# Performance work log

Measured on AMD Instinct MI355X. Metric: run time of the kernel, lower is better.

Reference implementation:

```python
import jax, jax.numpy as jnp
import numpy as np

N, H, W, CIN, COUT, FSIZE = 8, 128, 128, 64, 128, 3
EPS = 1e-3      # keras BatchNormalization default epsilon
ALPHA = 0.2     # LeakyReLU alpha


def setup_inputs() -> dict:
    key = jax.random.key(0)
    k0, k1, k2 = jax.random.split(key, 3)
    return {
        "inputs_real": jax.random.normal(k0, (N, H, W, CIN), jnp.float32),
        "inputs_imag": jax.random.normal(k1, (N, H, W, CIN), jnp.float32),
        "filters": jax.random.normal(k2, (FSIZE, FSIZE, CIN, COUT), jnp.float32) * 0.1,
        "gamma_real": jnp.ones((COUT,), jnp.float32),
        "beta_real": jnp.zeros((COUT,), jnp.float32),
        "gamma_imag": jnp.ones((COUT,), jnp.float32),
        "beta_imag": jnp.zeros((COUT,), jnp.float32),
    }


def _bn_train(x, gamma, beta):
    # BatchNorm in training mode: batch stats over (N, H, W), biased variance.
    mean = jnp.mean(x, axis=(0, 1, 2), keepdims=True)
    var = jnp.var(x, axis=(0, 1, 2), keepdims=True)
    return gamma * (x - mean) * jax.lax.rsqrt(var + EPS) + beta


def _leaky(x):
    return jnp.where(x >= 0, x, ALPHA * x)


def _spectral_kernels(filters):
    # Pad spatial filters [f,f,Cin,Cout] to [H,W,Cin,Cout] (bottom/right), FFT over H,W.
    f = filters.shape[0]
    fp = jnp.pad(filters, ((0, H - f), (0, W - f), (0, 0), (0, 0)))
    ff = jnp.fft.fft2(jnp.transpose(fp, (2, 3, 0, 1)).astype(jnp.complex64))  # [Cin,Cout,H,W]
    ff = jnp.transpose(ff, (2, 3, 0, 1))  # [H,W,Cin,Cout]
    kr = jnp.real(ff)
    ki = jnp.real(ff)  # faithful to source: filters_imag is ALSO tf.math.real(filters_freq)
    return kr, ki


def reference(inputs_real, inputs_imag, filters, gamma_real, beta_real, gamma_imag, beta_imag):
    kr, ki = _spectral_kernels(filters)
    # Fused form of the per-batch loop: sum over Cin of (ac+bd) and (bc-ad).
    out_real = (jnp.einsum('nhwc,hwco->nhwo', inputs_real, kr)
                + jnp.einsum('nhwc,hwco->nhwo', inputs_imag, ki))
    out_imag = (jnp.einsum('nhwc,hwco->nhwo', inputs_imag, kr)
                - jnp.einsum('nhwc,hwco->nhwo', inputs_real, ki))
    out_real = _leaky(_bn_train(out_real, gamma_real, beta_real))
    out_imag = _leaky(_bn_train(out_imag, gamma_imag, beta_imag))
    return (out_real, out_imag)
```

## Files before the change

### kernel.cpp

```cpp
#include <hip/hip_runtime.h>
#include <hip/hip_bf16.h>


typedef __bf16 bf16x8 __attribute__((ext_vector_type(8)));
typedef float f32x4 __attribute__((ext_vector_type(4)));

#define PQ_STRIDE   72
#define PQ_PLANE    (128 * PQ_STRIDE)
#define XS_STRIDE   72
#define XS_NP       (16 * XS_STRIDE)

__device__ __forceinline__ unsigned short f2bf(float x) {
    unsigned u = __float_as_uint(x);
    return (unsigned short)((u + 0x7FFFu + ((u >> 16) & 1u)) >> 16);
}
__device__ __forceinline__ unsigned pack2(float a, float b) {
    __hip_bfloat162 h = __float22bfloat162_rn(make_float2(a, b));
    return *reinterpret_cast<unsigned*>(&h);
}
__device__ __forceinline__ void unpack8(uint4 u, float* f) {
    f[0] = __uint_as_float(u.x << 16); f[1] = __uint_as_float(u.x & 0xffff0000u);
    f[2] = __uint_as_float(u.y << 16); f[3] = __uint_as_float(u.y & 0xffff0000u);
    f[4] = __uint_as_float(u.z << 16); f[5] = __uint_as_float(u.z & 0xffff0000u);
    f[6] = __uint_as_float(u.w << 16); f[7] = __uint_as_float(u.w & 0xffff0000u);
}

__global__ __launch_bounds__(512, 2) void conv_stats(
    const float* __restrict__ xr, const float* __restrict__ xi,
    const float* __restrict__ filt, float* __restrict__ out,
    float* __restrict__ gstats)
{
    __shared__ __align__(16) unsigned short pqT[5 * PQ_PLANE];
    __shared__ __align__(16) unsigned short xsh[16 * XS_NP];
    __shared__ float statl[512];

    const int t = threadIdx.x;
    const int u = blockIdx.x >> 3;
    const int vbase = (blockIdx.x & 7) * 16;

    const float au = 6.28318530717958647692f * (float)u / 128.0f;
    float su1, cu1, su2, cu2;
    __sincosf(au, &su1, &cu1);
    __sincosf(2.0f * au, &su2, &cu2);
    unsigned* pq32 = (unsigned*)pqT;

    #pragma unroll
    for (int k = 0; k < 8; ++k) {
        int i = t + k * 512;
        int o = i & 127;
        int cp = i >> 7;
        int g0 = (2 * cp) * 128 + o;
        int g1 = g0 + 128;
        unsigned widx = o * 36 + cp;
        #pragma unroll
        for (int b = 0; b < 3; ++b) {
            float f0a = filt[b * 8192 + g0],        f0b = filt[b * 8192 + g1];
            float f1a = filt[(3 + b) * 8192 + g0],  f1b = filt[(3 + b) * 8192 + g1];
            float f2a = filt[(6 + b) * 8192 + g0],  f2b = filt[(6 + b) * 8192 + g1];
            float Pa = f0a + cu1 * f1a + cu2 * f2a;
            float Pb = f0b + cu1 * f1b + cu2 * f2b;
            pq32[b * 4608 + widx] = pack2(Pa, Pb);
            if (b > 0) {
                float Qa = su1 * f1a + su2 * f2a;
                float Qb = su1 * f1b + su2 * f2b;
                pq32[(b + 2) * 4608 + widx] = pack2(Qa, Qb);
            }
        }
    }

    #pragma unroll
    for (int k = 0; k < 16; ++k) {
        int p = t + k * 512;
        int c = p & 63;
        int v = (p >> 6) & 15;
        int n = p >> 10;
        size_t gi = ((size_t)(n * 128 + u) * 128 + (size_t)(vbase + v)) * 64 + c;
        float r = xr[gi], im = xi[gi];
        xsh[v * XS_NP + n * XS_STRIDE + c]       = f2bf(r + im);
        xsh[v * XS_NP + (8 + n) * XS_STRIDE + c] = f2bf(im - r);
    }
    __syncthreads();

    const int wave = t >> 6;
    const int lane = t & 63;
    const int vg   = wave >> 1;
    const int nth  = wave & 1;
    const int ln15 = lane & 15;
    const int q    = lane >> 4;

    float cv1[4], cv2[4], nsv1[4], nsv2[4];
    #pragma unroll
    for (int vj = 0; vj < 4; ++vj) {
        float av = 6.28318530717958647692f * (float)(vbase + vg * 4 + vj) / 128.0f;
        float s1, c1, s2, c2;
        __sincosf(av, &s1, &c1);
        __sincosf(2.0f * av, &s2, &c2);
        cv1[vj] = c1; cv2[vj] = c2; nsv1[vj] = -s1; nsv2[vj] = -s2;
    }

    bf16x8 af[4][2];
    #pragma unroll
    for (int vj = 0; vj < 4; ++vj) {
        const unsigned short* xrow = &xsh[(vg * 4 + vj) * XS_NP + ln15 * XS_STRIDE];
        af[vj][0] = __builtin_bit_cast(bf16x8, *(const uint4*)(xrow + q * 8));
        af[vj][1] = __builtin_bit_cast(bf16x8, *(const uint4*)(xrow + 32 + q * 8));
    }

    f32x4 acc[4][4];
    #pragma unroll
    for (int vj = 0; vj < 4; ++vj)
        #pragma unroll
        for (int ntl = 0; ntl < 4; ++ntl)
            acc[vj][ntl] = (f32x4){0.f, 0.f, 0.f, 0.f};

    #pragma unroll
    for (int ntl = 0; ntl < 4; ++ntl) {
        const int o = (nth * 4 + ntl) * 16 + ln15;
        const unsigned short* prow = &pqT[o * PQ_STRIDE];
        #pragma unroll
        for (int ks = 0; ks < 2; ++ks) {
            const int coff = ks * 32 + q * 8;
            float P0[8], P1[8], P2[8], Q1[8], Q2[8];
            unpack8(*(const uint4*)(prow + 0 * PQ_PLANE + coff), P0);
            unpack8(*(const uint4*)(prow + 1 * PQ_PLANE + coff), P1);
            unpack8(*(const uint4*)(prow + 2 * PQ_PLANE + coff), P2);
            unpack8(*(const uint4*)(prow + 3 * PQ_PLANE + coff), Q1);
            unpack8(*(const uint4*)(prow + 4 * PQ_PLANE + coff), Q2);
            #pragma unroll
            for (int vj = 0; vj < 4; ++vj) {
                float kr[8];
                #pragma unroll
                for (int j = 0; j < 8; ++j) {
                    float tv = fmaf(cv1[vj], P1[j], P0[j]);
                    tv = fmaf(cv2[vj], P2[j], tv);
                    tv = fmaf(nsv1[vj], Q1[j], tv);
                    kr[j] = fmaf(nsv2[vj], Q2[j], tv);
                }
                uint4 B;
                B.x = pack2(kr[0], kr[1]); B.y = pack2(kr[2], kr[3]);
                B.z = pack2(kr[4], kr[5]); B.w = pack2(kr[6], kr[7]);
                acc[vj][ntl] = __builtin_amdgcn_mfma_f32_16x16x32_bf16(
                    af[vj][ks], __builtin_bit_cast(bf16x8, B), acc[vj][ntl], 0, 0, 0);
            }
        }
    }

    float ssum[4] = {0, 0, 0, 0}, ssq[4] = {0, 0, 0, 0};
    const int part = q >> 1;
    const int nbase = (q & 1) * 4;
    #pragma unroll
    for (int vj = 0; vj < 4; ++vj) {
        const int v = vbase + vg * 4 + vj;
        const size_t pos = ((size_t)(u * 128 + v)) * 128;
        #pragma unroll
        for (int ntl = 0; ntl < 4; ++ntl) {
            const int o = (nth * 4 + ntl) * 16 + ln15;
            size_t base = (size_t)part * 16777216 + (size_t)nbase * 2097152 + pos + o;
            #pragma unroll
            for (int r = 0; r < 4; ++r) {
                float y = acc[vj][ntl][r];
                __builtin_nontemporal_store(y, out + base + (size_t)r * 2097152);
                ssum[ntl] += y;
                ssq[ntl] = fmaf(y, y, ssq[ntl]);
            }
        }
    }

    statl[t] = 0.f;
    __syncthreads();
    #pragma unroll
    for (int ntl = 0; ntl < 4; ++ntl) {
        int ch = part * 128 + (nth * 4 + ntl) * 16 + ln15;
        atomicAdd(&statl[ch], ssum[ntl]);
        atomicAdd(&statl[256 + ch], ssq[ntl]);
    }
    __syncthreads();
    atomicAdd(&gstats[t], statl[t]);
}

__global__ void bn_prep(const float* __restrict__ gstats,
                        const float* __restrict__ gr, const float* __restrict__ br,
                        const float* __restrict__ gi, const float* __restrict__ bi,
                        float* __restrict__ sc_sh)
{
    int t = threadIdx.x;
    if (t < 256) {
        int part = t >> 7, o = t & 127;
        const float inv = 1.0f / 131072.0f;
        float mean = gstats[t] * inv;
        float var  = gstats[256 + t] * inv - mean * mean;
        float g = part ? gi[o] : gr[o];
        float b = part ? bi[o] : br[o];
        float s = g * rsqrtf(var + 1e-3f);
        sc_sh[t]       = s;
        sc_sh[256 + t] = b - mean * s;
    }
}

__global__ __launch_bounds__(256) void bn_apply(float* __restrict__ out,
                                                const float* __restrict__ sc_sh)
{
    size_t base = (size_t)blockIdx.x * 256 + threadIdx.x;
    #pragma unroll
    for (int it = 0; it < 4; ++it, base += (size_t)8192 * 256) {
        size_t e = base * 4;
        int part = (int)(e >> 24);
        int o = (int)(e & 127);
        const f32x4 sc = *(const f32x4*)(sc_sh + part * 128 + o);
        const f32x4 sh = *(const f32x4*)(sc_sh + 256 + part * 128 + o);
        f32x4 x = __builtin_nontemporal_load((const f32x4*)(out + e));
        f32x4 y;
        y[0] = fmaf(x[0], sc[0], sh[0]);
        y[1] = fmaf(x[1], sc[1], sh[1]);
        y[2] = fmaf(x[2], sc[2], sh[2]);
        y[3] = fmaf(x[3], sc[3], sh[3]);
        x[0] = y[0] >= 0.0f ? y[0] : 0.2f * y[0];
        x[1] = y[1] >= 0.0f ? y[1] : 0.2f * y[1];
        x[2] = y[2] >= 0.0f ? y[2] : 0.2f * y[2];
        x[3] = y[3] >= 0.0f ? y[3] : 0.2f * y[3];
        __builtin_nontemporal_store(x, (f32x4*)(out + e));
    }
}

extern "C" void kernel_launch(void* const* d_in, const int* in_sizes, int n_in,
                              void* d_out, int out_size, void* d_ws, size_t ws_size,
                              hipStream_t stream)
{
    const float* xr   = (const float*)d_in[0];
    const float* xi   = (const float*)d_in[1];
    const float* filt = (const float*)d_in[2];
    const float* gr   = (const float*)d_in[3];
    const float* br   = (const float*)d_in[4];
    const float* gi   = (const float*)d_in[5];
    const float* bi   = (const float*)d_in[6];
    float* out = (float*)d_out;
    float* ws  = (float*)d_ws;

    (void)hipMemsetAsync(ws, 0, 512 * sizeof(float), stream);
    conv_stats<<<dim3(1024), dim3(512), 0, stream>>>(xr, xi, filt, out, ws);
    bn_prep<<<dim3(1), dim3(256), 0, stream>>>(ws, gr, br, gi, bi, ws + 512);
    bn_apply<<<dim3(8192), dim3(256), 0, stream>>>(out, ws + 512);
}
```

Baseline: 299.7 us.

## Split output channels per block, loop over v-chunks with swizzled LDS

Blocks now cover half the output channels (64) and a 64-wide strip of v, looping over four 16-wide v chunks. The per-u filter P/Q planes are built once per block and reused across chunks. Input tiles are staged with vector float2 loads into an XOR-swizzled LDS layout instead of padded strides, so LDS use drops and launch bounds allow 4 blocks per CU. Nontemporal stores and loads are replaced with ordinary ones. The trade-off is half as many blocks, a sync per chunk, and each input tile being loaded by both channel-half blocks.

```diff
diff --git a/kernel.cpp b/kernel.cpp
--- a/kernel.cpp
+++ b/kernel.cpp
@@ -5,15 +5,6 @@
 typedef __bf16 bf16x8 __attribute__((ext_vector_type(8)));
 typedef float f32x4 __attribute__((ext_vector_type(4)));
 
-#define PQ_STRIDE   72
-#define PQ_PLANE    (128 * PQ_STRIDE)
-#define XS_STRIDE   72
-#define XS_NP       (16 * XS_STRIDE)
-
-__device__ __forceinline__ unsigned short f2bf(float x) {
-    unsigned u = __float_as_uint(x);
-    return (unsigned short)((u + 0x7FFFu + ((u >> 16) & 1u)) >> 16);
-}
 __device__ __forceinline__ unsigned pack2(float a, float b) {
     __hip_bfloat162 h = __float22bfloat162_rn(make_float2(a, b));
     return *reinterpret_cast<unsigned*>(&h);
@@ -25,61 +16,54 @@
     f[6] = __uint_as_float(u.w << 16); f[7] = __uint_as_float(u.w & 0xffff0000u);
 }
 
-__global__ __launch_bounds__(512, 2) void conv_stats(
+__global__ __launch_bounds__(512, 4) void conv_stats(
     const float* __restrict__ xr, const float* __restrict__ xi,
     const float* __restrict__ filt, float* __restrict__ out,
     float* __restrict__ gstats)
 {
-    __shared__ __align__(16) unsigned short pqT[5 * PQ_PLANE];
-    __shared__ __align__(16) unsigned short xsh[16 * XS_NP];
+    __shared__ __align__(16) unsigned short pqT[5 * 4096];
+    __shared__ __align__(16) unsigned short xsh[16 * 16 * 64];
     __shared__ float statl[512];
 
     const int t = threadIdx.x;
-    const int u = blockIdx.x >> 3;
-    const int vbase = (blockIdx.x & 7) * 16;
+    const int gid = blockIdx.x;
+    const int oh = gid >> 8;
+    const int u  = (gid & 255) >> 1;
+    const int vh = gid & 1;
+    const int obase = oh << 6;
+    const int vbase0 = vh << 6;
+
+    unsigned* pq32 = (unsigned*)pqT;
+    unsigned* xs32 = (unsigned*)xsh;
 
     const float au = 6.28318530717958647692f * (float)u / 128.0f;
     float su1, cu1, su2, cu2;
     __sincosf(au, &su1, &cu1);
     __sincosf(2.0f * au, &su2, &cu2);
-    unsigned* pq32 = (unsigned*)pqT;
 
     #pragma unroll
-    for (int k = 0; k < 8; ++k) {
+    for (int k = 0; k < 4; ++k) {
         int i = t + k * 512;
-        int o = i & 127;
-        int cp = i >> 7;
-        int g0 = (2 * cp) * 128 + o;
+        int o = i & 63;
+        int cp = i >> 6;
+        int g0 = (2 * cp) * 128 + obase + o;
         int g1 = g0 + 128;
-        unsigned widx = o * 36 + cp;
+        unsigned wd = o * 32 + (((cp >> 2) ^ (o & 7)) << 2) + (cp & 3);
         #pragma unroll
         for (int b = 0; b < 3; ++b) {
-            float f0a = filt[b * 8192 + g0],        f0b = filt[b * 8192 + g1];
-            float f1a = filt[(3 + b) * 8192 + g0],  f1b = filt[(3 + b) * 8192 + g1];
-            float f2a = filt[(6 + b) * 8192 + g0],  f2b = filt[(6 + b) * 8192 + g1];
-            float Pa = f0a + cu1 * f1a + cu2 * f2a;
-            float Pb = f0b + cu1 * f1b + cu2 * f2b;
-            pq32[b * 4608 + widx] = pack2(Pa, Pb);
+            float f0a = filt[b * 8192 + g0],       f0b = filt[b * 8192 + g1];
+            float f1a = filt[(3 + b) * 8192 + g0], f1b = filt[(3 + b) * 8192 + g1];
+            float f2a = filt[(6 + b) * 8192 + g0], f2b = filt[(6 + b) * 8192 + g1];
+            float Pa = fmaf(cu2, f2a, fmaf(cu1, f1a, f0a));
+            float Pb = fmaf(cu2, f2b, fmaf(cu1, f1b, f0b));
+            pq32[b * 2048 + wd] = pack2(Pa, Pb);
             if (b > 0) {
-                float Qa = su1 * f1a + su2 * f2a;
-                float Qb = su1 * f1b + su2 * f2b;
-                pq32[(b + 2) * 4608 + widx] = pack2(Qa, Qb);
-            }
-        }
-    }
-
-    #pragma unroll
-    for (int k = 0; k < 16; ++k) {
-        int p = t + k * 512;
-        int c = p & 63;
-        int v = (p >> 6) & 15;
-        int n = p >> 10;
-        size_t gi = ((size_t)(n * 128 + u) * 128 + (size_t)(vbase + v)) * 64 + c;
-        float r = xr[gi], im = xi[gi];
-        xsh[v * XS_NP + n * XS_STRIDE + c]       = f2bf(r + im);
-        xsh[v * XS_NP + (8 + n) * XS_STRIDE + c] = f2bf(im - r);
-    }
-    __syncthreads();
+                float Qa = fmaf(su2, f2a, su1 * f1a);
+                float Qb = fmaf(su2, f2b, su1 * f1b);
+                pq32[(b + 2) * 2048 + wd] = pack2(Qa, Qb);
+            }
+        }
+    }
 
     const int wave = t >> 6;
     const int lane = t & 63;
@@ -87,92 +71,120 @@
     const int nth  = wave & 1;
     const int ln15 = lane & 15;
     const int q    = lane >> 4;
-
-    float cv1[4], cv2[4], nsv1[4], nsv2[4];
-    #pragma unroll
-    for (int vj = 0; vj < 4; ++vj) {
-        float av = 6.28318530717958647692f * (float)(vbase + vg * 4 + vj) / 128.0f;
-        float s1, c1, s2, c2;
-        __sincosf(av, &s1, &c1);
-        __sincosf(2.0f * av, &s2, &c2);
-        cv1[vj] = c1; cv2[vj] = c2; nsv1[vj] = -s1; nsv2[vj] = -s2;
-    }
-
-    bf16x8 af[4][2];
-    #pragma unroll
-    for (int vj = 0; vj < 4; ++vj) {
-        const unsigned short* xrow = &xsh[(vg * 4 + vj) * XS_NP + ln15 * XS_STRIDE];
-        af[vj][0] = __builtin_bit_cast(bf16x8, *(const uint4*)(xrow + q * 8));
-        af[vj][1] = __builtin_bit_cast(bf16x8, *(const uint4*)(xrow + 32 + q * 8));
-    }
-
-    f32x4 acc[4][4];
-    #pragma unroll
-    for (int vj = 0; vj < 4; ++vj)
-        #pragma unroll
-        for (int ntl = 0; ntl < 4; ++ntl)
-            acc[vj][ntl] = (f32x4){0.f, 0.f, 0.f, 0.f};
-
-    #pragma unroll
-    for (int ntl = 0; ntl < 4; ++ntl) {
-        const int o = (nth * 4 + ntl) * 16 + ln15;
-        const unsigned short* prow = &pqT[o * PQ_STRIDE];
-        #pragma unroll
-        for (int ks = 0; ks < 2; ++ks) {
-            const int coff = ks * 32 + q * 8;
-            float P0[8], P1[8], P2[8], Q1[8], Q2[8];
-            unpack8(*(const uint4*)(prow + 0 * PQ_PLANE + coff), P0);
-            unpack8(*(const uint4*)(prow + 1 * PQ_PLANE + coff), P1);
-            unpack8(*(const uint4*)(prow + 2 * PQ_PLANE + coff), P2);
-            unpack8(*(const uint4*)(prow + 3 * PQ_PLANE + coff), Q1);
-            unpack8(*(const uint4*)(prow + 4 * PQ_PLANE + coff), Q2);
-            #pragma unroll
-            for (int vj = 0; vj < 4; ++vj) {
-                float kr[8];
-                #pragma unroll
-                for (int j = 0; j < 8; ++j) {
-                    float tv = fmaf(cv1[vj], P1[j], P0[j]);
-                    tv = fmaf(cv2[vj], P2[j], tv);
-                    tv = fmaf(nsv1[vj], Q1[j], tv);
-                    kr[j] = fmaf(nsv2[vj], Q2[j], tv);
-                }
-                uint4 B;
-                B.x = pack2(kr[0], kr[1]); B.y = pack2(kr[2], kr[3]);
-                B.z = pack2(kr[4], kr[5]); B.w = pack2(kr[6], kr[7]);
-                acc[vj][ntl] = __builtin_amdgcn_mfma_f32_16x16x32_bf16(
-                    af[vj][ks], __builtin_bit_cast(bf16x8, B), acc[vj][ntl], 0, 0, 0);
-            }
-        }
-    }
-
-    float ssum[4] = {0, 0, 0, 0}, ssq[4] = {0, 0, 0, 0};
+    const int swz  = ln15 & 7;
     const int part = q >> 1;
     const int nbase = (q & 1) * 4;
-    #pragma unroll
-    for (int vj = 0; vj < 4; ++vj) {
-        const int v = vbase + vg * 4 + vj;
-        const size_t pos = ((size_t)(u * 128 + v)) * 128;
-        #pragma unroll
-        for (int ntl = 0; ntl < 4; ++ntl) {
-            const int o = (nth * 4 + ntl) * 16 + ln15;
-            size_t base = (size_t)part * 16777216 + (size_t)nbase * 2097152 + pos + o;
-            #pragma unroll
-            for (int r = 0; r < 4; ++r) {
-                float y = acc[vj][ntl][r];
-                __builtin_nontemporal_store(y, out + base + (size_t)r * 2097152);
-                ssum[ntl] += y;
-                ssq[ntl] = fmaf(y, y, ssq[ntl]);
-            }
-        }
+
+    const int sv = t >> 5;
+    const int scp = t & 31;
+
+    float ssum[2] = {0.f, 0.f}, ssq[2] = {0.f, 0.f};
+
+    #pragma unroll 1
+    for (int ch = 0; ch < 4; ++ch) {
+        {
+            const int vglob = vbase0 + ch * 16 + sv;
+            unsigned wb = (sv * 16) * 32 + (((scp >> 2) ^ 0) << 2) + (scp & 3);
+            #pragma unroll
+            for (int n = 0; n < 8; ++n) {
+                size_t gi = (((size_t)(n * 128 + u)) * 128 + vglob) * 64 + 2 * scp;
+                float2 r  = *(const float2*)(xr + gi);
+                float2 m2 = *(const float2*)(xi + gi);
+                unsigned rp = pack2(r.x + m2.x, r.y + m2.y);
+                unsigned ip = pack2(m2.x - r.x, m2.y - r.y);
+                unsigned base = (sv * 16 + n) * 32 + (((scp >> 2) ^ (n & 7)) << 2) + (scp & 3);
+                xs32[base] = rp;
+                xs32[base + 8 * 32] = ip;
+            }
+            (void)wb;
+        }
+        __syncthreads();
+
+        float cv1[4], cv2[4], nsv1[4], nsv2[4];
+        #pragma unroll
+        for (int vj = 0; vj < 4; ++vj) {
+            float av = 6.28318530717958647692f *
+                       (float)(vbase0 + ch * 16 + vg * 4 + vj) / 128.0f;
+            float s1, c1, s2, c2;
+            __sincosf(av, &s1, &c1);
+            __sincosf(2.0f * av, &s2, &c2);
+            cv1[vj] = c1; cv2[vj] = c2; nsv1[vj] = -s1; nsv2[vj] = -s2;
+        }
+
+        bf16x8 af[4][2];
+        #pragma unroll
+        for (int vj = 0; vj < 4; ++vj) {
+            const unsigned short* xrow = &xsh[((vg * 4 + vj) * 16 + ln15) * 64];
+            #pragma unroll
+            for (int ks = 0; ks < 2; ++ks) {
+                int m = ks * 4 + q;
+                af[vj][ks] = __builtin_bit_cast(bf16x8,
+                    *(const uint4*)(xrow + ((m ^ swz) << 3)));
+            }
+        }
+
+        #pragma unroll
+        for (int ntl = 0; ntl < 2; ++ntl) {
+            const int ot = nth * 2 + ntl;
+            const int o_loc = ot * 16 + ln15;
+            const unsigned short* prow = &pqT[o_loc * 64];
+            f32x4 acc[4];
+            #pragma unroll
+            for (int vj = 0; vj < 4; ++vj) acc[vj] = (f32x4){0.f, 0.f, 0.f, 0.f};
+
+            #pragma unroll
+            for (int ks = 0; ks < 2; ++ks) {
+                const int m = ks * 4 + q;
+                const int foff = (m ^ swz) << 3;
+                float P0[8], P1[8], P2[8], Q1[8], Q2[8];
+                unpack8(*(const uint4*)(prow + 0 * 4096 + foff), P0);
+                unpack8(*(const uint4*)(prow + 1 * 4096 + foff), P1);
+                unpack8(*(const uint4*)(prow + 2 * 4096 + foff), P2);
+                unpack8(*(const uint4*)(prow + 3 * 4096 + foff), Q1);
+                unpack8(*(const uint4*)(prow + 4 * 4096 + foff), Q2);
+                #pragma unroll
+                for (int vj = 0; vj < 4; ++vj) {
+                    float kr[8];
+                    #pragma unroll
+                    for (int j = 0; j < 8; ++j) {
+                        float tv = fmaf(cv1[vj], P1[j], P0[j]);
+                        tv = fmaf(cv2[vj], P2[j], tv);
+                        tv = fmaf(nsv1[vj], Q1[j], tv);
+                        kr[j] = fmaf(nsv2[vj], Q2[j], tv);
+                    }
+                    uint4 B;
+                    B.x = pack2(kr[0], kr[1]); B.y = pack2(kr[2], kr[3]);
+                    B.z = pack2(kr[4], kr[5]); B.w = pack2(kr[6], kr[7]);
+                    acc[vj] = __builtin_amdgcn_mfma_f32_16x16x32_bf16(
+                        af[vj][ks], __builtin_bit_cast(bf16x8, B), acc[vj], 0, 0, 0);
+                }
+            }
+
+            const int o_glob = obase + o_loc;
+            #pragma unroll
+            for (int vj = 0; vj < 4; ++vj) {
+                const int vglob = vbase0 + ch * 16 + vg * 4 + vj;
+                size_t base = (size_t)part * 16777216 + (size_t)nbase * 2097152
+                            + ((size_t)(u * 128 + vglob)) * 128 + o_glob;
+                #pragma unroll
+                for (int r = 0; r < 4; ++r) {
+                    float y = acc[vj][r];
+                    out[base + (size_t)r * 2097152] = y;
+                    ssum[ntl] += y;
+                    ssq[ntl] = fmaf(y, y, ssq[ntl]);
+                }
+            }
+        }
+        __syncthreads();
     }
 
     statl[t] = 0.f;
     __syncthreads();
     #pragma unroll
-    for (int ntl = 0; ntl < 4; ++ntl) {
-        int ch = part * 128 + (nth * 4 + ntl) * 16 + ln15;
-        atomicAdd(&statl[ch], ssum[ntl]);
-        atomicAdd(&statl[256 + ch], ssq[ntl]);
+    for (int ntl = 0; ntl < 2; ++ntl) {
+        int chn = part * 128 + obase + (nth * 2 + ntl) * 16 + ln15;
+        atomicAdd(&statl[chn], ssum[ntl]);
+        atomicAdd(&statl[256 + chn], ssq[ntl]);
     }
     __syncthreads();
     atomicAdd(&gstats[t], statl[t]);
@@ -208,7 +220,7 @@
         int o = (int)(e & 127);
         const f32x4 sc = *(const f32x4*)(sc_sh + part * 128 + o);
         const f32x4 sh = *(const f32x4*)(sc_sh + 256 + part * 128 + o);
-        f32x4 x = __builtin_nontemporal_load((const f32x4*)(out + e));
+        f32x4 x = *(const f32x4*)(out + e);
         f32x4 y;
         y[0] = fmaf(x[0], sc[0], sh[0]);
         y[1] = fmaf(x[1], sc[1], sh[1]);
@@ -237,7 +249,7 @@
     float* ws  = (float*)d_ws;
 
     (void)hipMemsetAsync(ws, 0, 512 * sizeof(float), stream);
-    conv_stats<<<dim3(1024), dim3(512), 0, stream>>>(xr, xi, filt, out, ws);
+    conv_stats<<<dim3(512), dim3(512), 0, stream>>>(xr, xi, filt, out, ws);
     bn_prep<<<dim3(1), dim3(256), 0, stream>>>(ws, gr, br, gi, bi, ws + 512);
     bn_apply<<<dim3(8192), dim3(256), 0, stream>>>(out, ws + 512);
 }
```

New measurement: 311.2 us. 3.8% more time.
